# Kernel tuning notes

Hardware: AMD Instinct MI355X
Metric: run time of the kernel (lower is better)

## Reference

```python
import jax, jax.numpy as jnp
import numpy as np

D_MODEL = 1024
N_HEADS = 16
HEAD_DIM = D_MODEL // N_HEADS


def setup_inputs() -> dict:
    key = jax.random.key(0)
    ks = jax.random.split(key, 5)
    x = jax.random.normal(ks[0], (2, 2048, D_MODEL), dtype=jnp.float32)
    s = 1.0 / np.sqrt(D_MODEL)
    W_qkv = jax.random.normal(ks[1], (D_MODEL, 3 * D_MODEL), dtype=jnp.float32) * s
    b_qkv = jnp.zeros((3 * D_MODEL,), dtype=jnp.float32)
    W_proj = jax.random.normal(ks[2], (D_MODEL, D_MODEL), dtype=jnp.float32) * s
    b_proj = jnp.zeros((D_MODEL,), dtype=jnp.float32)
    return {"x": x, "W_qkv": W_qkv, "b_qkv": b_qkv, "W_proj": W_proj, "b_proj": b_proj}


def reference(x, W_qkv, b_qkv, W_proj, b_proj):
    b, t, c = x.shape
    qkv = x @ W_qkv + b_qkv  # [b,t,3c]
    q, k, v = jnp.split(qkv, 3, axis=-1)
    # [b, h, t, d]
    q = q.reshape(b, t, N_HEADS, HEAD_DIM).transpose(0, 2, 1, 3)
    k = k.reshape(b, t, N_HEADS, HEAD_DIM).transpose(0, 2, 1, 3)
    v = v.reshape(b, t, N_HEADS, HEAD_DIM).transpose(0, 2, 1, 3)
    att = jnp.einsum('bhqd,bhkd->bhqk', q, k) / np.sqrt(HEAD_DIM)
    causal = jnp.tril(jnp.ones((t, t), dtype=bool))  # [t,t]
    att = jnp.where(causal[None, None], att, -jnp.inf)
    att = jax.nn.softmax(att, axis=-1)
    out = jnp.einsum('bhqk,bhkd->bhqd', att, v)  # [b,h,t,d]
    out = out.transpose(0, 2, 1, 3).reshape(b, t, c)
    return out @ W_proj + b_proj
```

## Files before the change

### kernel.cpp

```cpp
#include <hip/hip_runtime.h>
#include <hip/hip_bf16.h>

#define NB 2
#define NH 16
#define HD 64
#define DM 1024
#define TT 2048

typedef __attribute__((ext_vector_type(4))) float f32x4;
typedef __attribute__((ext_vector_type(8))) short bf16x8;

__device__ __forceinline__ unsigned short f2bf(float f) {
  union { float f; unsigned int i; } x; x.f = f;
  unsigned int r = x.i + 0x7fffu + ((x.i >> 16) & 1u);
  return (unsigned short)(r >> 16);
}

__device__ __forceinline__ unsigned int cvtpk(float lo, float hi) {
  unsigned int r;
  asm("v_cvt_pk_bf16_f32 %0, %1, %2" : "=v"(r) : "v"(lo), "v"(hi));
  return r;
}

__device__ __forceinline__ void async16(unsigned short* lds_base, const unsigned short* g) {
  __builtin_amdgcn_global_load_lds(
      (const __attribute__((address_space(1))) void*)g,
      (__attribute__((address_space(3))) void*)lds_base, 16, 0, 0);
}

__global__ __launch_bounds__(256)
void convert_bf16_kernel(const float* __restrict__ in, unsigned short* __restrict__ out, int n8)
{
  const int i = blockIdx.x * 256 + threadIdx.x;
  if (i >= n8) return;
  const f32x4 a = *(const f32x4*)(in + (size_t)i * 8);
  const f32x4 b = *(const f32x4*)(in + (size_t)i * 8 + 4);
  uint4 o;
  o.x = f2bf(a.x) | ((unsigned)f2bf(a.y) << 16);
  o.y = f2bf(a.z) | ((unsigned)f2bf(a.w) << 16);
  o.z = f2bf(b.x) | ((unsigned)f2bf(b.y) << 16);
  o.w = f2bf(b.z) | ((unsigned)f2bf(b.w) << 16);
  *(uint4*)(out + (size_t)i * 8) = o;
}

__global__ __launch_bounds__(256)
void transpose_convert(const float* __restrict__ W, unsigned short* __restrict__ WT,
                       int K, int N)
{
  __shared__ unsigned short T[64][72];
  const int t = threadIdx.x;
  const int k0 = blockIdx.y * 64, n0 = blockIdx.x * 64;
  const int r = t >> 2;
  const int c = (t & 3) * 16;
  const float* src = W + (size_t)(k0 + r) * N + n0 + c;
  #pragma unroll
  for (int s = 0; s < 4; ++s) {
    const f32x4 v = *(const f32x4*)(src + s * 4);
    T[c + s*4 + 0][r] = f2bf(v.x);
    T[c + s*4 + 1][r] = f2bf(v.y);
    T[c + s*4 + 2][r] = f2bf(v.z);
    T[c + s*4 + 3][r] = f2bf(v.w);
  }
  __syncthreads();
  unsigned short* dst = WT + (size_t)(n0 + r) * K + k0 + c;
  *(uint4*)(dst)     = *(const uint4*)(&T[r][c]);
  *(uint4*)(dst + 8) = *(const uint4*)(&T[r][c + 8]);
}

template<int MODE>
__global__ __launch_bounds__(256)
void gemm_bf16(const unsigned short* __restrict__ A, const unsigned short* __restrict__ BT,
               const float* __restrict__ bias, void* __restrict__ Cout,
               int M, int N, int K)
{
  __shared__ unsigned short As[128 * 32];
  __shared__ unsigned short Bs[128 * 32];
  const int tid = threadIdx.x;
  const int lane = tid & 63;
  const int w = tid >> 6;
  const int wr = w >> 1, wc = w & 1;
  const int l15 = lane & 15, g = lane >> 4;
  const int m0 = blockIdx.y * 128;
  const int n0 = blockIdx.x * 128;

  f32x4 acc[4][4] = {};

  const int ar0 = tid >> 2,          as0 = (tid & 3) * 8;
  const int ar1 = (256 + tid) >> 2;
  const unsigned short* A0 = A + (size_t)(m0 + ar0) * K + as0;
  const unsigned short* A1 = A + (size_t)(m0 + ar1) * K + as0;
  const unsigned short* B0 = BT + (size_t)(n0 + ar0) * K + as0;
  const unsigned short* B1 = BT + (size_t)(n0 + ar1) * K + as0;
  unsigned short* AsW0 = &As[(0 * 256 + w * 64) * 8];
  unsigned short* AsW1 = &As[(1 * 256 + w * 64) * 8];
  unsigned short* BsW0 = &Bs[(0 * 256 + w * 64) * 8];
  unsigned short* BsW1 = &Bs[(1 * 256 + w * 64) * 8];

  for (int k0 = 0; k0 < K; k0 += 32) {
    async16(AsW0, A0 + k0);
    async16(AsW1, A1 + k0);
    async16(BsW0, B0 + k0);
    async16(BsW1, B1 + k0);
    __syncthreads();

    bf16x8 af[4], bfv[4];
    #pragma unroll
    for (int i = 0; i < 4; ++i)
      af[i] = *(const bf16x8*)(&As[(wr * 64 + i * 16 + l15) * 32 + g * 8]);
    #pragma unroll
    for (int j = 0; j < 4; ++j)
      bfv[j] = *(const bf16x8*)(&Bs[(wc * 64 + j * 16 + l15) * 32 + g * 8]);
    #pragma unroll
    for (int i = 0; i < 4; ++i)
      #pragma unroll
      for (int j = 0; j < 4; ++j)
        acc[i][j] = __builtin_amdgcn_mfma_f32_16x16x32_bf16(af[i], bfv[j], acc[i][j], 0, 0, 0);
    __syncthreads();
  }

  #pragma unroll
  for (int i = 0; i < 4; ++i) {
    #pragma unroll
    for (int j = 0; j < 4; ++j) {
      #pragma unroll
      for (int e = 0; e < 4; ++e) {
        const int row = m0 + wr * 64 + i * 16 + g * 4 + e;
        const int col = n0 + wc * 64 + j * 16 + l15;
        float val = acc[i][j][e] + bias[col];
        if (MODE == 0) {
          const int which = col >> 10;
          if (which == 0) val *= 0.125f;
          const int rem = col & 1023;
          const int hh = rem >> 6, dd = rem & 63;
          const int bb = row >> 11, tt = row & 2047;
          ((unsigned short*)Cout)[((((size_t)which * NB + bb) * NH + hh) * TT + tt) * HD + dd] = f2bf(val);
        } else {
          ((float*)Cout)[(size_t)row * N + col] = val;
        }
      }
    }
  }
}

__global__ __launch_bounds__(512)
void attn_kernel(const unsigned short* __restrict__ qkv, unsigned short* __restrict__ attn_out)
{
  __shared__ unsigned short Ksm[64 * 72];
  __shared__ unsigned short VTsm[64 * 70];
  __shared__ unsigned short Psm[8][32 * 72];

  const int tid = threadIdx.x;
  const int lane = tid & 63;
  const int wv = tid >> 6;
  const int l15 = lane & 15;
  const int g = lane >> 4;

  const int li = blockIdx.x;
  const int xcd = li & 7;
  const int j = li >> 3;
  const int bh = ((j >> 3) << 3) | xcd;
  const int ip = j & 7;

  const int qlo0 = ip * 128;
  const int qhi0 = (15 - ip) * 128;

  const size_t base = (size_t)bh * TT * HD;
  const unsigned short* Qg = qkv + base;
  const unsigned short* Kg = qkv + (size_t)NB * NH * TT * HD + base;
  const unsigned short* Vg = qkv + (size_t)2 * NB * NH * TT * HD + base;

  const int qw_lo = qlo0 + wv * 16;
  const int qw_hi = qhi0 + wv * 16;
  const bf16x8 qlf0 = *(const bf16x8*)(Qg + (size_t)(qw_lo + l15) * HD + g * 8);
  const bf16x8 qlf1 = *(const bf16x8*)(Qg + (size_t)(qw_lo + l15) * HD + 32 + g * 8);
  const bf16x8 qhf0 = *(const bf16x8*)(Qg + (size_t)(qw_hi + l15) * HD + g * 8);
  const bf16x8 qhf1 = *(const bf16x8*)(Qg + (size_t)(qw_hi + l15) * HD + 32 + g * 8);

  f32x4 olo[4] = {}, ohi[4] = {};
  float llo = 0.f, lhi = 0.f;

  const bool kRole = (wv < 4);
  const int krow = (tid & 255) >> 2;
  const int kseg = (tid & 3) * 16;
  const int vt   = tid & 255;
  const int vr0  = (vt >> 4) * 4;
  const int vc0  = (vt & 15) * 4;

  const int nt    = 32 - 2 * ip;
  const int lo_nt = 2 * ip + 2;

  uint4 st0, st1;
  {
    if (kRole) {
      const unsigned short* kp = Kg + (size_t)krow * HD + kseg;
      st0 = *(const uint4*)(kp);
      st1 = *(const uint4*)(kp + 8);
    } else {
      const uint2 a = *(const uint2*)(Vg + (size_t)(vr0 + 0) * HD + vc0);
      const uint2 b = *(const uint2*)(Vg + (size_t)(vr0 + 1) * HD + vc0);
      const uint2 c = *(const uint2*)(Vg + (size_t)(vr0 + 2) * HD + vc0);
      const uint2 d = *(const uint2*)(Vg + (size_t)(vr0 + 3) * HD + vc0);
      st0.x = a.x; st0.y = a.y; st0.z = b.x; st0.w = b.y;
      st1.x = c.x; st1.y = c.y; st1.z = d.x; st1.w = d.y;
    }
  }

  for (int t = 0; t < nt; ++t) {
    const int t0 = t * 64;
    const bool lo_act = (t < lo_nt);
    __syncthreads();
    if (kRole) {
      *(uint4*)(&Ksm[krow * 72 + kseg])     = st0;
      *(uint4*)(&Ksm[krow * 72 + kseg + 8]) = st1;
    } else {
      unsigned short r0[4] = {(unsigned short)(st0.x & 0xffffu), (unsigned short)(st0.x >> 16),
                              (unsigned short)(st0.y & 0xffffu), (unsigned short)(st0.y >> 16)};
      unsigned short r1[4] = {(unsigned short)(st0.z & 0xffffu), (unsigned short)(st0.z >> 16),
                              (unsigned short)(st0.w & 0xffffu), (unsigned short)(st0.w >> 16)};
      unsigned short r2[4] = {(unsigned short)(st1.x & 0xffffu), (unsigned short)(st1.x >> 16),
                              (unsigned short)(st1.y & 0xffffu), (unsigned short)(st1.y >> 16)};
      unsigned short r3[4] = {(unsigned short)(st1.z & 0xffffu), (unsigned short)(st1.z >> 16),
                              (unsigned short)(st1.w & 0xffffu), (unsigned short)(st1.w >> 16)};
      #pragma unroll
      for (int c = 0; c < 4; ++c) {
        ushort4 col;
        col.x = r0[c]; col.y = r1[c]; col.z = r2[c]; col.w = r3[c];
        *(ushort4*)(&VTsm[(vc0 + c) * 70 + vr0]) = col;
      }
    }
    __syncthreads();

    if (t + 1 < nt) {
      const int t1 = t0 + 64;
      if (kRole) {
        const unsigned short* kp = Kg + (size_t)(t1 + krow) * HD + kseg;
        st0 = *(const uint4*)(kp);
        st1 = *(const uint4*)(kp + 8);
      } else {
        const uint2 a = *(const uint2*)(Vg + (size_t)(t1 + vr0 + 0) * HD + vc0);
        const uint2 b = *(const uint2*)(Vg + (size_t)(t1 + vr0 + 1) * HD + vc0);
        const uint2 c = *(const uint2*)(Vg + (size_t)(t1 + vr0 + 2) * HD + vc0);
        const uint2 d = *(const uint2*)(Vg + (size_t)(t1 + vr0 + 3) * HD + vc0);
        st0.x = a.x; st0.y = a.y; st0.z = b.x; st0.w = b.y;
        st1.x = c.x; st1.y = c.y; st1.z = d.x; st1.w = d.y;
      }
    }

    f32x4 shiT[4] = {}, sloT[4] = {};
    __builtin_amdgcn_s_setprio(1);
    #pragma unroll
    for (int b = 0; b < 4; ++b) {
      const bf16x8 kf0 = *(const bf16x8*)(&Ksm[(b * 16 + l15) * 72 + g * 8]);
      const bf16x8 kf1 = *(const bf16x8*)(&Ksm[(b * 16 + l15) * 72 + 32 + g * 8]);
      shiT[b] = __builtin_amdgcn_mfma_f32_16x16x32_bf16(kf0, qhf0, shiT[b], 0, 0, 0);
      shiT[b] = __builtin_amdgcn_mfma_f32_16x16x32_bf16(kf1, qhf1, shiT[b], 0, 0, 0);
      if (lo_act) {
        sloT[b] = __builtin_amdgcn_mfma_f32_16x16x32_bf16(kf0, qlf0, sloT[b], 0, 0, 0);
        sloT[b] = __builtin_amdgcn_mfma_f32_16x16x32_bf16(kf1, qlf1, sloT[b], 0, 0, 0);
      }
    }
    __builtin_amdgcn_s_setprio(0);

    if (t0 + 63 > qw_hi) {
      #pragma unroll
      for (int b = 0; b < 4; ++b)
        #pragma unroll
        for (int e = 0; e < 4; ++e)
          if (t0 + b * 16 + 4 * g + e > qw_hi + l15) shiT[b][e] = -INFINITY;
    }
    if (lo_act && t0 + 63 > qw_lo) {
      #pragma unroll
      for (int b = 0; b < 4; ++b)
        #pragma unroll
        for (int e = 0; e < 4; ++e)
          if (t0 + b * 16 + 4 * g + e > qw_lo + l15) sloT[b][e] = -INFINITY;
    }

    #pragma unroll
    for (int b = 0; b < 4; ++b) {
      const float p0 = __expf(shiT[b][0]);
      const float p1 = __expf(shiT[b][1]);
      const float p2 = __expf(shiT[b][2]);
      const float p3 = __expf(shiT[b][3]);
      lhi += (p0 + p1) + (p2 + p3);
      uint2 wd; wd.x = cvtpk(p0, p1); wd.y = cvtpk(p2, p3);
      *(uint2*)(&Psm[wv][(16 + l15) * 72 + b * 16 + 4 * g]) = wd;
    }
    if (lo_act) {
      #pragma unroll
      for (int b = 0; b < 4; ++b) {
        const float p0 = __expf(sloT[b][0]);
        const float p1 = __expf(sloT[b][1]);
        const float p2 = __expf(sloT[b][2]);
        const float p3 = __expf(sloT[b][3]);
        llo += (p0 + p1) + (p2 + p3);
        uint2 wd; wd.x = cvtpk(p0, p1); wd.y = cvtpk(p2, p3);
        *(uint2*)(&Psm[wv][l15 * 72 + b * 16 + 4 * g]) = wd;
      }
    }

    __builtin_amdgcn_s_setprio(1);
    #pragma unroll
    for (int c = 0; c < 2; ++c) {
      const bf16x8 pfh = *(const bf16x8*)(&Psm[wv][(16 + l15) * 72 + c * 32 + g * 8]);
      bf16x8 pfl;
      if (lo_act) pfl = *(const bf16x8*)(&Psm[wv][l15 * 72 + c * 32 + g * 8]);
      #pragma unroll
      for (int db = 0; db < 4; ++db) {
        const bf16x8 vf = *(const bf16x8*)(&VTsm[(db * 16 + l15) * 70 + c * 32 + g * 8]);
        ohi[db] = __builtin_amdgcn_mfma_f32_16x16x32_bf16(pfh, vf, ohi[db], 0, 0, 0);
        if (lo_act) olo[db] = __builtin_amdgcn_mfma_f32_16x16x32_bf16(pfl, vf, olo[db], 0, 0, 0);
      }
    }
    __builtin_amdgcn_s_setprio(0);
  }

  lhi += __shfl_xor(lhi, 16, 64);
  lhi += __shfl_xor(lhi, 32, 64);
  llo += __shfl_xor(llo, 16, 64);
  llo += __shfl_xor(llo, 32, 64);

  const int bb = bh >> 4;
  const int hh = bh & 15;
  #pragma unroll
  for (int e = 0; e < 4; ++e) {
    const float invh = 1.f / __shfl(lhi, 4 * g + e, 64);
    const float invl = 1.f / __shfl(llo, 4 * g + e, 64);
    const int qh = qw_hi + 4 * g + e;
    const int ql = qw_lo + 4 * g + e;
    #pragma unroll
    for (int db = 0; db < 4; ++db) {
      attn_out[(size_t)(bb * TT + qh) * DM + hh * HD + db * 16 + l15] = f2bf(ohi[db][e] * invh);
      attn_out[(size_t)(bb * TT + ql) * DM + hh * HD + db * 16 + l15] = f2bf(olo[db][e] * invl);
    }
  }
}

extern "C" void kernel_launch(void* const* d_in, const int* in_sizes, int n_in,
                              void* d_out, int out_size, void* d_ws, size_t ws_size,
                              hipStream_t stream)
{
  const float* x     = (const float*)d_in[0];
  const float* Wqkv  = (const float*)d_in[1];
  const float* bqkv  = (const float*)d_in[2];
  const float* Wproj = (const float*)d_in[3];
  const float* bproj = (const float*)d_in[4];

  const size_t qkv_elems = (size_t)3 * NB * NH * TT * HD;
  unsigned short* qkv_ws  = (unsigned short*)d_ws;
  unsigned short* WqkvT   = qkv_ws + qkv_elems;
  unsigned short* WprojT  = WqkvT + (size_t)3 * DM * DM;
  unsigned short* xbf     = WprojT + (size_t)DM * DM;
  unsigned short* attn_ws = xbf;

  hipLaunchKernelGGL(convert_bf16_kernel, dim3((NB * TT * DM / 8 + 255) / 256, 1, 1), dim3(256), 0, stream,
                     x, xbf, NB * TT * DM / 8);
  hipLaunchKernelGGL(transpose_convert, dim3(3 * DM / 64, DM / 64, 1), dim3(256), 0, stream,
                     Wqkv, WqkvT, DM, 3 * DM);
  hipLaunchKernelGGL(transpose_convert, dim3(DM / 64, DM / 64, 1), dim3(256), 0, stream,
                     Wproj, WprojT, DM, DM);
  hipLaunchKernelGGL((gemm_bf16<0>), dim3(3 * DM / 128, NB * TT / 128, 1), dim3(256), 0, stream,
                     xbf, WqkvT, bqkv, (void*)qkv_ws, NB * TT, 3 * DM, DM);
  hipLaunchKernelGGL(attn_kernel, dim3(256, 1, 1), dim3(512), 0, stream,
                     qkv_ws, attn_ws);
  hipLaunchKernelGGL((gemm_bf16<1>), dim3(DM / 128, NB * TT / 128, 1), dim3(256), 0, stream,
                     attn_ws, WprojT, bproj, d_out, NB * TT, DM, DM);
}
```

Before: 141.4 us.

## Double-buffer K/V tiles in attention and swizzle GEMM tiles across XCDs

```diff
diff --git a/kernel.cpp b/kernel.cpp
--- a/kernel.cpp
+++ b/kernel.cpp
@@ -80,8 +80,13 @@
   const int w = tid >> 6;
   const int wr = w >> 1, wc = w & 1;
   const int l15 = lane & 15, g = lane >> 4;
-  const int m0 = blockIdx.y * 128;
-  const int n0 = blockIdx.x * 128;
+
+  const int gx = gridDim.x;
+  const int li = blockIdx.y * gx + blockIdx.x;
+  const int chunk = (gx * gridDim.y) >> 3;
+  const int tile = (li & 7) * chunk + (li >> 3);
+  const int m0 = (tile / gx) * 128;
+  const int n0 = (tile % gx) * 128;
 
   f32x4 acc[4][4] = {};
 
@@ -145,9 +150,9 @@
 __global__ __launch_bounds__(512)
 void attn_kernel(const unsigned short* __restrict__ qkv, unsigned short* __restrict__ attn_out)
 {
-  __shared__ unsigned short Ksm[64 * 72];
-  __shared__ unsigned short VTsm[64 * 70];
-  __shared__ unsigned short Psm[8][32 * 72];
+  __shared__ unsigned short Ksm[2][64 * 66];
+  __shared__ unsigned short VTsm[2][64 * 70];
+  __shared__ unsigned short Psm[8][32 * 66];
 
   const int tid = threadIdx.x;
   const int lane = tid & 63;
@@ -190,47 +195,43 @@
   const int lo_nt = 2 * ip + 2;
 
   uint4 st0, st1;
-  {
-    if (kRole) {
-      const unsigned short* kp = Kg + (size_t)krow * HD + kseg;
-      st0 = *(const uint4*)(kp);
-      st1 = *(const uint4*)(kp + 8);
-    } else {
-      const uint2 a = *(const uint2*)(Vg + (size_t)(vr0 + 0) * HD + vc0);
-      const uint2 b = *(const uint2*)(Vg + (size_t)(vr0 + 1) * HD + vc0);
-      const uint2 c = *(const uint2*)(Vg + (size_t)(vr0 + 2) * HD + vc0);
-      const uint2 d = *(const uint2*)(Vg + (size_t)(vr0 + 3) * HD + vc0);
-      st0.x = a.x; st0.y = a.y; st0.z = b.x; st0.w = b.y;
-      st1.x = c.x; st1.y = c.y; st1.z = d.x; st1.w = d.y;
-    }
-  }
-
+  if (kRole) {
+    const unsigned short* kp = Kg + (size_t)krow * HD + kseg;
+    st0 = *(const uint4*)(kp);
+    st1 = *(const uint4*)(kp + 8);
+    *(uint4*)(&Ksm[0][krow * 66 + kseg])     = st0;
+    *(uint4*)(&Ksm[0][krow * 66 + kseg + 8]) = st1;
+  } else {
+    const uint2 a = *(const uint2*)(Vg + (size_t)(vr0 + 0) * HD + vc0);
+    const uint2 b = *(const uint2*)(Vg + (size_t)(vr0 + 1) * HD + vc0);
+    const uint2 c = *(const uint2*)(Vg + (size_t)(vr0 + 2) * HD + vc0);
+    const uint2 d = *(const uint2*)(Vg + (size_t)(vr0 + 3) * HD + vc0);
+    st0.x = a.x; st0.y = a.y; st0.z = b.x; st0.w = b.y;
+    st1.x = c.x; st1.y = c.y; st1.z = d.x; st1.w = d.y;
+    unsigned short r0[4] = {(unsigned short)(st0.x & 0xffffu), (unsigned short)(st0.x >> 16),
+                            (unsigned short)(st0.y & 0xffffu), (unsigned short)(st0.y >> 16)};
+    unsigned short r1[4] = {(unsigned short)(st0.z & 0xffffu), (unsigned short)(st0.z >> 16),
+                            (unsigned short)(st0.w & 0xffffu), (unsigned short)(st0.w >> 16)};
+    unsigned short r2[4] = {(unsigned short)(st1.x & 0xffffu), (unsigned short)(st1.x >> 16),
+                            (unsigned short)(st1.y & 0xffffu), (unsigned short)(st1.y >> 16)};
+    unsigned short r3[4] = {(unsigned short)(st1.z & 0xffffu), (unsigned short)(st1.z >> 16),
+                            (unsigned short)(st1.w & 0xffffu), (unsigned short)(st1.w >> 16)};
+    #pragma unroll
+    for (int c2 = 0; c2 < 4; ++c2) {
+      ushort4 col;
+      col.x = r0[c2]; col.y = r1[c2]; col.z = r2[c2]; col.w = r3[c2];
+      *(ushort4*)(&VTsm[0][(vc0 + c2) * 70 + vr0]) = col;
+    }
+  }
+
+  int cur = 0;
   for (int t = 0; t < nt; ++t) {
     const int t0 = t * 64;
     const bool lo_act = (t < lo_nt);
+    const bool pre = (t + 1 < nt);
     __syncthreads();
-    if (kRole) {
-      *(uint4*)(&Ksm[krow * 72 + kseg])     = st0;
-      *(uint4*)(&Ksm[krow * 72 + kseg + 8]) = st1;
-    } else {
-      unsigned short r0[4] = {(unsigned short)(st0.x & 0xffffu), (unsigned short)(st0.x >> 16),
-                              (unsigned short)(st0.y & 0xffffu), (unsigned short)(st0.y >> 16)};
-      unsigned short r1[4] = {(unsigned short)(st0.z & 0xffffu), (unsigned short)(st0.z >> 16),
-                              (unsigned short)(st0.w & 0xffffu), (unsigned short)(st0.w >> 16)};
-      unsigned short r2[4] = {(unsigned short)(st1.x & 0xffffu), (unsigned short)(st1.x >> 16),
-                              (unsigned short)(st1.y & 0xffffu), (unsigned short)(st1.y >> 16)};
-      unsigned short r3[4] = {(unsigned short)(st1.z & 0xffffu), (unsigned short)(st1.z >> 16),
-                              (unsigned short)(st1.w & 0xffffu), (unsigned short)(st1.w >> 16)};
-      #pragma unroll
-      for (int c = 0; c < 4; ++c) {
-        ushort4 col;
-        col.x = r0[c]; col.y = r1[c]; col.z = r2[c]; col.w = r3[c];
-        *(ushort4*)(&VTsm[(vc0 + c) * 70 + vr0]) = col;
-      }
-    }
-    __syncthreads();
-
-    if (t + 1 < nt) {
+
+    if (pre) {
       const int t1 = t0 + 64;
       if (kRole) {
         const unsigned short* kp = Kg + (size_t)(t1 + krow) * HD + kseg;
@@ -246,12 +247,15 @@
       }
     }
 
+    const unsigned short* kb = Ksm[cur];
+    const unsigned short* vb = VTsm[cur];
+
     f32x4 shiT[4] = {}, sloT[4] = {};
     __builtin_amdgcn_s_setprio(1);
     #pragma unroll
     for (int b = 0; b < 4; ++b) {
-      const bf16x8 kf0 = *(const bf16x8*)(&Ksm[(b * 16 + l15) * 72 + g * 8]);
-      const bf16x8 kf1 = *(const bf16x8*)(&Ksm[(b * 16 + l15) * 72 + 32 + g * 8]);
+      const bf16x8 kf0 = *(const bf16x8*)(&kb[(b * 16 + l15) * 66 + g * 8]);
+      const bf16x8 kf1 = *(const bf16x8*)(&kb[(b * 16 + l15) * 66 + 32 + g * 8]);
       shiT[b] = __builtin_amdgcn_mfma_f32_16x16x32_bf16(kf0, qhf0, shiT[b], 0, 0, 0);
       shiT[b] = __builtin_amdgcn_mfma_f32_16x16x32_bf16(kf1, qhf1, shiT[b], 0, 0, 0);
       if (lo_act) {
@@ -284,7 +288,7 @@
       const float p3 = __expf(shiT[b][3]);
       lhi += (p0 + p1) + (p2 + p3);
       uint2 wd; wd.x = cvtpk(p0, p1); wd.y = cvtpk(p2, p3);
-      *(uint2*)(&Psm[wv][(16 + l15) * 72 + b * 16 + 4 * g]) = wd;
+      *(uint2*)(&Psm[wv][(16 + l15) * 66 + b * 16 + 4 * g]) = wd;
     }
     if (lo_act) {
       #pragma unroll
@@ -295,24 +299,47 @@
         const float p3 = __expf(sloT[b][3]);
         llo += (p0 + p1) + (p2 + p3);
         uint2 wd; wd.x = cvtpk(p0, p1); wd.y = cvtpk(p2, p3);
-        *(uint2*)(&Psm[wv][l15 * 72 + b * 16 + 4 * g]) = wd;
+        *(uint2*)(&Psm[wv][l15 * 66 + b * 16 + 4 * g]) = wd;
       }
     }
 
     __builtin_amdgcn_s_setprio(1);
     #pragma unroll
     for (int c = 0; c < 2; ++c) {
-      const bf16x8 pfh = *(const bf16x8*)(&Psm[wv][(16 + l15) * 72 + c * 32 + g * 8]);
+      const bf16x8 pfh = *(const bf16x8*)(&Psm[wv][(16 + l15) * 66 + c * 32 + g * 8]);
       bf16x8 pfl;
-      if (lo_act) pfl = *(const bf16x8*)(&Psm[wv][l15 * 72 + c * 32 + g * 8]);
+      if (lo_act) pfl = *(const bf16x8*)(&Psm[wv][l15 * 66 + c * 32 + g * 8]);
       #pragma unroll
       for (int db = 0; db < 4; ++db) {
-        const bf16x8 vf = *(const bf16x8*)(&VTsm[(db * 16 + l15) * 70 + c * 32 + g * 8]);
+        const bf16x8 vf = *(const bf16x8*)(&vb[(db * 16 + l15) * 70 + c * 32 + g * 8]);
         ohi[db] = __builtin_amdgcn_mfma_f32_16x16x32_bf16(pfh, vf, ohi[db], 0, 0, 0);
         if (lo_act) olo[db] = __builtin_amdgcn_mfma_f32_16x16x32_bf16(pfl, vf, olo[db], 0, 0, 0);
       }
     }
     __builtin_amdgcn_s_setprio(0);
+
+    if (pre) {
+      if (kRole) {
+        *(uint4*)(&Ksm[cur ^ 1][krow * 66 + kseg])     = st0;
+        *(uint4*)(&Ksm[cur ^ 1][krow * 66 + kseg + 8]) = st1;
+      } else {
+        unsigned short r0[4] = {(unsigned short)(st0.x & 0xffffu), (unsigned short)(st0.x >> 16),
+                                (unsigned short)(st0.y & 0xffffu), (unsigned short)(st0.y >> 16)};
+        unsigned short r1[4] = {(unsigned short)(st0.z & 0xffffu), (unsigned short)(st0.z >> 16),
+                                (unsigned short)(st0.w & 0xffffu), (unsigned short)(st0.w >> 16)};
+        unsigned short r2[4] = {(unsigned short)(st1.x & 0xffffu), (unsigned short)(st1.x >> 16),
+                                (unsigned short)(st1.y & 0xffffu), (unsigned short)(st1.y >> 16)};
+        unsigned short r3[4] = {(unsigned short)(st1.z & 0xffffu), (unsigned short)(st1.z >> 16),
+                                (unsigned short)(st1.w & 0xffffu), (unsigned short)(st1.w >> 16)};
+        #pragma unroll
+        for (int c2 = 0; c2 < 4; ++c2) {
+          ushort4 col;
+          col.x = r0[c2]; col.y = r1[c2]; col.z = r2[c2]; col.w = r3[c2];
+          *(ushort4*)(&VTsm[cur ^ 1][(vc0 + c2) * 70 + vr0]) = col;
+        }
+      }
+    }
+    cur ^= 1;
   }
 
   lhi += __shfl_xor(lhi, 16, 64);
```

New measurement: 223.9 us. 1.58x slower.

## Stage two KV tiles per barrier in attention and swizzle GEMM tiles across XCDs

Applied to the files above, without the earlier changes.

```diff
diff --git a/kernel.cpp b/kernel.cpp
--- a/kernel.cpp
+++ b/kernel.cpp
@@ -80,8 +80,13 @@
   const int w = tid >> 6;
   const int wr = w >> 1, wc = w & 1;
   const int l15 = lane & 15, g = lane >> 4;
-  const int m0 = blockIdx.y * 128;
-  const int n0 = blockIdx.x * 128;
+
+  const int gx = gridDim.x;
+  const int li = blockIdx.y * gx + blockIdx.x;
+  const int chunk = (gx * gridDim.y) >> 3;
+  const int tile = (li & 7) * chunk + (li >> 3);
+  const int m0 = (tile / gx) * 128;
+  const int n0 = (tile % gx) * 128;
 
   f32x4 acc[4][4] = {};
 
@@ -145,8 +150,8 @@
 __global__ __launch_bounds__(512)
 void attn_kernel(const unsigned short* __restrict__ qkv, unsigned short* __restrict__ attn_out)
 {
-  __shared__ unsigned short Ksm[64 * 72];
-  __shared__ unsigned short VTsm[64 * 70];
+  __shared__ unsigned short Ksm[2][64 * 72];
+  __shared__ unsigned short VTsm[2][64 * 70];
   __shared__ unsigned short Psm[8][32 * 72];
 
   const int tid = threadIdx.x;
@@ -186,133 +191,149 @@
   const int vr0  = (vt >> 4) * 4;
   const int vc0  = (vt & 15) * 4;
 
-  const int nt    = 32 - 2 * ip;
+  const int nt2   = 16 - ip;
   const int lo_nt = 2 * ip + 2;
 
-  uint4 st0, st1;
-  {
+  uint4 stA[2], stB[2];
+  #pragma unroll
+  for (int h = 0; h < 2; ++h) {
+    const int k0g = h * 64;
     if (kRole) {
-      const unsigned short* kp = Kg + (size_t)krow * HD + kseg;
-      st0 = *(const uint4*)(kp);
-      st1 = *(const uint4*)(kp + 8);
+      const unsigned short* kp = Kg + (size_t)(k0g + krow) * HD + kseg;
+      stA[h] = *(const uint4*)(kp);
+      stB[h] = *(const uint4*)(kp + 8);
     } else {
-      const uint2 a = *(const uint2*)(Vg + (size_t)(vr0 + 0) * HD + vc0);
-      const uint2 b = *(const uint2*)(Vg + (size_t)(vr0 + 1) * HD + vc0);
-      const uint2 c = *(const uint2*)(Vg + (size_t)(vr0 + 2) * HD + vc0);
-      const uint2 d = *(const uint2*)(Vg + (size_t)(vr0 + 3) * HD + vc0);
-      st0.x = a.x; st0.y = a.y; st0.z = b.x; st0.w = b.y;
-      st1.x = c.x; st1.y = c.y; st1.z = d.x; st1.w = d.y;
-    }
-  }
-
-  for (int t = 0; t < nt; ++t) {
-    const int t0 = t * 64;
-    const bool lo_act = (t < lo_nt);
+      const uint2 a = *(const uint2*)(Vg + (size_t)(k0g + vr0 + 0) * HD + vc0);
+      const uint2 b = *(const uint2*)(Vg + (size_t)(k0g + vr0 + 1) * HD + vc0);
+      const uint2 c = *(const uint2*)(Vg + (size_t)(k0g + vr0 + 2) * HD + vc0);
+      const uint2 d = *(const uint2*)(Vg + (size_t)(k0g + vr0 + 3) * HD + vc0);
+      stA[h].x = a.x; stA[h].y = a.y; stA[h].z = b.x; stA[h].w = b.y;
+      stB[h].x = c.x; stB[h].y = c.y; stB[h].z = d.x; stB[h].w = d.y;
+    }
+  }
+
+  for (int T = 0; T < nt2; ++T) {
     __syncthreads();
-    if (kRole) {
-      *(uint4*)(&Ksm[krow * 72 + kseg])     = st0;
-      *(uint4*)(&Ksm[krow * 72 + kseg + 8]) = st1;
-    } else {
-      unsigned short r0[4] = {(unsigned short)(st0.x & 0xffffu), (unsigned short)(st0.x >> 16),
-                              (unsigned short)(st0.y & 0xffffu), (unsigned short)(st0.y >> 16)};
-      unsigned short r1[4] = {(unsigned short)(st0.z & 0xffffu), (unsigned short)(st0.z >> 16),
-                              (unsigned short)(st0.w & 0xffffu), (unsigned short)(st0.w >> 16)};
-      unsigned short r2[4] = {(unsigned short)(st1.x & 0xffffu), (unsigned short)(st1.x >> 16),
-                              (unsigned short)(st1.y & 0xffffu), (unsigned short)(st1.y >> 16)};
-      unsigned short r3[4] = {(unsigned short)(st1.z & 0xffffu), (unsigned short)(st1.z >> 16),
-                              (unsigned short)(st1.w & 0xffffu), (unsigned short)(st1.w >> 16)};
-      #pragma unroll
-      for (int c = 0; c < 4; ++c) {
-        ushort4 col;
-        col.x = r0[c]; col.y = r1[c]; col.z = r2[c]; col.w = r3[c];
-        *(ushort4*)(&VTsm[(vc0 + c) * 70 + vr0]) = col;
+    #pragma unroll
+    for (int h = 0; h < 2; ++h) {
+      if (kRole) {
+        *(uint4*)(&Ksm[h][krow * 72 + kseg])     = stA[h];
+        *(uint4*)(&Ksm[h][krow * 72 + kseg + 8]) = stB[h];
+      } else {
+        unsigned short r0[4] = {(unsigned short)(stA[h].x & 0xffffu), (unsigned short)(stA[h].x >> 16),
+                                (unsigned short)(stA[h].y & 0xffffu), (unsigned short)(stA[h].y >> 16)};
+        unsigned short r1[4] = {(unsigned short)(stA[h].z & 0xffffu), (unsigned short)(stA[h].z >> 16),
+                                (unsigned short)(stA[h].w & 0xffffu), (unsigned short)(stA[h].w >> 16)};
+        unsigned short r2[4] = {(unsigned short)(stB[h].x & 0xffffu), (unsigned short)(stB[h].x >> 16),
+                                (unsigned short)(stB[h].y & 0xffffu), (unsigned short)(stB[h].y >> 16)};
+        unsigned short r3[4] = {(unsigned short)(stB[h].z & 0xffffu), (unsigned short)(stB[h].z >> 16),
+                                (unsigned short)(stB[h].w & 0xffffu), (unsigned short)(stB[h].w >> 16)};
+        #pragma unroll
+        for (int c2 = 0; c2 < 4; ++c2) {
+          ushort4 col;
+          col.x = r0[c2]; col.y = r1[c2]; col.z = r2[c2]; col.w = r3[c2];
+          *(ushort4*)(&VTsm[h][(vc0 + c2) * 70 + vr0]) = col;
+        }
       }
     }
     __syncthreads();
 
-    if (t + 1 < nt) {
-      const int t1 = t0 + 64;
-      if (kRole) {
-        const unsigned short* kp = Kg + (size_t)(t1 + krow) * HD + kseg;
-        st0 = *(const uint4*)(kp);
-        st1 = *(const uint4*)(kp + 8);
-      } else {
-        const uint2 a = *(const uint2*)(Vg + (size_t)(t1 + vr0 + 0) * HD + vc0);
-        const uint2 b = *(const uint2*)(Vg + (size_t)(t1 + vr0 + 1) * HD + vc0);
-        const uint2 c = *(const uint2*)(Vg + (size_t)(t1 + vr0 + 2) * HD + vc0);
-        const uint2 d = *(const uint2*)(Vg + (size_t)(t1 + vr0 + 3) * HD + vc0);
-        st0.x = a.x; st0.y = a.y; st0.z = b.x; st0.w = b.y;
-        st1.x = c.x; st1.y = c.y; st1.z = d.x; st1.w = d.y;
-      }
-    }
-
-    f32x4 shiT[4] = {}, sloT[4] = {};
-    __builtin_amdgcn_s_setprio(1);
-    #pragma unroll
-    for (int b = 0; b < 4; ++b) {
-      const bf16x8 kf0 = *(const bf16x8*)(&Ksm[(b * 16 + l15) * 72 + g * 8]);
-      const bf16x8 kf1 = *(const bf16x8*)(&Ksm[(b * 16 + l15) * 72 + 32 + g * 8]);
-      shiT[b] = __builtin_amdgcn_mfma_f32_16x16x32_bf16(kf0, qhf0, shiT[b], 0, 0, 0);
-      shiT[b] = __builtin_amdgcn_mfma_f32_16x16x32_bf16(kf1, qhf1, shiT[b], 0, 0, 0);
+    if (T + 1 < nt2) {
+      const int tb = (T + 1) * 128;
+      #pragma unroll
+      for (int h = 0; h < 2; ++h) {
+        const int k0g = tb + h * 64;
+        if (kRole) {
+          const unsigned short* kp = Kg + (size_t)(k0g + krow) * HD + kseg;
+          stA[h] = *(const uint4*)(kp);
+          stB[h] = *(const uint4*)(kp + 8);
+        } else {
+          const uint2 a = *(const uint2*)(Vg + (size_t)(k0g + vr0 + 0) * HD + vc0);
+          const uint2 b = *(const uint2*)(Vg + (size_t)(k0g + vr0 + 1) * HD + vc0);
+          const uint2 c = *(const uint2*)(Vg + (size_t)(k0g + vr0 + 2) * HD + vc0);
+          const uint2 d = *(const uint2*)(Vg + (size_t)(k0g + vr0 + 3) * HD + vc0);
+          stA[h].x = a.x; stA[h].y = a.y; stA[h].z = b.x; stA[h].w = b.y;
+          stB[h].x = c.x; stB[h].y = c.y; stB[h].z = d.x; stB[h].w = d.y;
+        }
+      }
+    }
+
+    #pragma unroll
+    for (int h = 0; h < 2; ++h) {
+      const int t64 = 2 * T + h;
+      const int t0 = t64 * 64;
+      const bool lo_act = (t64 < lo_nt);
+      const unsigned short* kb = Ksm[h];
+      const unsigned short* vb = VTsm[h];
+
+      f32x4 shiT[4] = {}, sloT[4] = {};
+      __builtin_amdgcn_s_setprio(1);
+      #pragma unroll
+      for (int b = 0; b < 4; ++b) {
+        const bf16x8 kf0 = *(const bf16x8*)(&kb[(b * 16 + l15) * 72 + g * 8]);
+        const bf16x8 kf1 = *(const bf16x8*)(&kb[(b * 16 + l15) * 72 + 32 + g * 8]);
+        shiT[b] = __builtin_amdgcn_mfma_f32_16x16x32_bf16(kf0, qhf0, shiT[b], 0, 0, 0);
+        shiT[b] = __builtin_amdgcn_mfma_f32_16x16x32_bf16(kf1, qhf1, shiT[b], 0, 0, 0);
+        if (lo_act) {
+          sloT[b] = __builtin_amdgcn_mfma_f32_16x16x32_bf16(kf0, qlf0, sloT[b], 0, 0, 0);
+          sloT[b] = __builtin_amdgcn_mfma_f32_16x16x32_bf16(kf1, qlf1, sloT[b], 0, 0, 0);
+        }
+      }
+      __builtin_amdgcn_s_setprio(0);
+
+      if (t0 + 63 > qw_hi) {
+        #pragma unroll
+        for (int b = 0; b < 4; ++b)
+          #pragma unroll
+          for (int e = 0; e < 4; ++e)
+            if (t0 + b * 16 + 4 * g + e > qw_hi + l15) shiT[b][e] = -INFINITY;
+      }
+      if (lo_act && t0 + 63 > qw_lo) {
+        #pragma unroll
+        for (int b = 0; b < 4; ++b)
+          #pragma unroll
+          for (int e = 0; e < 4; ++e)
+            if (t0 + b * 16 + 4 * g + e > qw_lo + l15) sloT[b][e] = -INFINITY;
+      }
+
+      #pragma unroll
+      for (int b = 0; b < 4; ++b) {
+        const float p0 = __expf(shiT[b][0]);
+        const float p1 = __expf(shiT[b][1]);
+        const float p2 = __expf(shiT[b][2]);
+        const float p3 = __expf(shiT[b][3]);
+        lhi += (p0 + p1) + (p2 + p3);
+        uint2 wd; wd.x = cvtpk(p0, p1); wd.y = cvtpk(p2, p3);
+        *(uint2*)(&Psm[wv][(16 + l15) * 72 + b * 16 + 4 * g]) = wd;
+      }
       if (lo_act) {
-        sloT[b] = __builtin_amdgcn_mfma_f32_16x16x32_bf16(kf0, qlf0, sloT[b], 0, 0, 0);
-        sloT[b] = __builtin_amdgcn_mfma_f32_16x16x32_bf16(kf1, qlf1, sloT[b], 0, 0, 0);
-      }
-    }
-    __builtin_amdgcn_s_setprio(0);
-
-    if (t0 + 63 > qw_hi) {
-      #pragma unroll
-      for (int b = 0; b < 4; ++b)
-        #pragma unroll
-        for (int e = 0; e < 4; ++e)
-          if (t0 + b * 16 + 4 * g + e > qw_hi + l15) shiT[b][e] = -INFINITY;
-    }
-    if (lo_act && t0 + 63 > qw_lo) {
-      #pragma unroll
-      for (int b = 0; b < 4; ++b)
-        #pragma unroll
-        for (int e = 0; e < 4; ++e)
-          if (t0 + b * 16 + 4 * g + e > qw_lo + l15) sloT[b][e] = -INFINITY;
-    }
-
-    #pragma unroll
-    for (int b = 0; b < 4; ++b) {
-      const float p0 = __expf(shiT[b][0]);
-      const float p1 = __expf(shiT[b][1]);
-      const float p2 = __expf(shiT[b][2]);
-      const float p3 = __expf(shiT[b][3]);
-      lhi += (p0 + p1) + (p2 + p3);
-      uint2 wd; wd.x = cvtpk(p0, p1); wd.y = cvtpk(p2, p3);
-      *(uint2*)(&Psm[wv][(16 + l15) * 72 + b * 16 + 4 * g]) = wd;
-    }
-    if (lo_act) {
-      #pragma unroll
-      for (int b = 0; b < 4; ++b) {
-        const float p0 = __expf(sloT[b][0]);
-        const float p1 = __expf(sloT[b][1]);
-        const float p2 = __expf(sloT[b][2]);
-        const float p3 = __expf(sloT[b][3]);
-        llo += (p0 + p1) + (p2 + p3);
-        uint2 wd; wd.x = cvtpk(p0, p1); wd.y = cvtpk(p2, p3);
-        *(uint2*)(&Psm[wv][l15 * 72 + b * 16 + 4 * g]) = wd;
-      }
-    }
-
-    __builtin_amdgcn_s_setprio(1);
-    #pragma unroll
-    for (int c = 0; c < 2; ++c) {
-      const bf16x8 pfh = *(const bf16x8*)(&Psm[wv][(16 + l15) * 72 + c * 32 + g * 8]);
-      bf16x8 pfl;
-      if (lo_act) pfl = *(const bf16x8*)(&Psm[wv][l15 * 72 + c * 32 + g * 8]);
-      #pragma unroll
-      for (int db = 0; db < 4; ++db) {
-        const bf16x8 vf = *(const bf16x8*)(&VTsm[(db * 16 + l15) * 70 + c * 32 + g * 8]);
-        ohi[db] = __builtin_amdgcn_mfma_f32_16x16x32_bf16(pfh, vf, ohi[db], 0, 0, 0);
-        if (lo_act) olo[db] = __builtin_amdgcn_mfma_f32_16x16x32_bf16(pfl, vf, olo[db], 0, 0, 0);
-      }
-    }
-    __builtin_amdgcn_s_setprio(0);
+        #pragma unroll
+        for (int b = 0; b < 4; ++b) {
+          const float p0 = __expf(sloT[b][0]);
+          const float p1 = __expf(sloT[b][1]);
+          const float p2 = __expf(sloT[b][2]);
+          const float p3 = __expf(sloT[b][3]);
+          llo += (p0 + p1) + (p2 + p3);
+          uint2 wd; wd.x = cvtpk(p0, p1); wd.y = cvtpk(p2, p3);
+          *(uint2*)(&Psm[wv][l15 * 72 + b * 16 + 4 * g]) = wd;
+        }
+      }
+
+      __builtin_amdgcn_s_setprio(1);
+      #pragma unroll
+      for (int c = 0; c < 2; ++c) {
+        const bf16x8 pfh = *(const bf16x8*)(&Psm[wv][(16 + l15) * 72 + c * 32 + g * 8]);
+        bf16x8 pfl;
+        if (lo_act) pfl = *(const bf16x8*)(&Psm[wv][l15 * 72 + c * 32 + g * 8]);
+        #pragma unroll
+        for (int db = 0; db < 4; ++db) {
+          const bf16x8 vf = *(const bf16x8*)(&vb[(db * 16 + l15) * 70 + c * 32 + g * 8]);
+          ohi[db] = __builtin_amdgcn_mfma_f32_16x16x32_bf16(pfh, vf, ohi[db], 0, 0, 0);
+          if (lo_act) olo[db] = __builtin_amdgcn_mfma_f32_16x16x32_bf16(pfl, vf, olo[db], 0, 0, 0);
+        }
+      }
+      __builtin_amdgcn_s_setprio(0);
+    }
   }
 
   lhi += __shfl_xor(lhi, 16, 64);
```

Result: slower. 175.3 us (+24.0%).
